# Optimization experiments

Measured on AMD Instinct MI355X. Metric: run time of the kernel, lower is better.

Reference implementation:

```python
import jax, jax.numpy as jnp
import numpy as np

N = 1024          # n_nodes
F = 32            # n_input_features (per-node embedding dim)
HID = 64          # n_hidden_features
OUT = 32          # n_output_features


def setup_inputs() -> dict:
    key = jax.random.key(0)
    k = jax.random.split(key, 7)
    Edges = jax.random.uniform(k[0], (N, N), dtype=jnp.float32)
    Coordinates = jax.random.normal(k[1], (N, 3), dtype=jnp.float32)
    Embeddings = jax.random.normal(k[2], (N, F), dtype=jnp.float32)
    # nn.Linear params: W (out, in), b (out,)
    s1 = 1.0 / np.sqrt(2 * F)
    s2 = 1.0 / np.sqrt(HID)
    W1 = jax.random.uniform(k[3], (HID, 2 * F), dtype=jnp.float32, minval=-s1, maxval=s1)
    b1 = jax.random.uniform(k[4], (HID,), dtype=jnp.float32, minval=-s1, maxval=s1)
    W2 = jax.random.uniform(k[5], (OUT, HID), dtype=jnp.float32, minval=-s2, maxval=s2)
    b2 = jax.random.uniform(k[6], (OUT,), dtype=jnp.float32, minval=-s2, maxval=s2)
    return {"Edges": Edges, "Coordinates": Coordinates, "Embeddings": Embeddings,
            "W1": W1, "b1": b1, "W2": W2, "b2": b2}


def _swish(x):
    return x * jax.nn.sigmoid(x)


def reference(Edges, Coordinates, Embeddings, W1, b1, W2, b2):
    # pairwise euclidean distances (torch.cdist p=2), grad-safe on the zero diagonal
    diff = Coordinates[:, None, :] - Coordinates[None, :, :]          # (N, N, 3)
    sq = jnp.sum(diff * diff, axis=-1)                                # (N, N)
    dist = jnp.where(sq > 0, jnp.sqrt(jnp.where(sq > 0, sq, 1.0)), 0.0)
    w = Edges * dist                                                  # (N, N)

    # H[i, j] = concat(Emb[i], Emb[j]); first Linear applied without
    # materializing the (N, N, 2F) tensor:
    # (w * [h_i, h_j]) @ W1^T = w * (h_i @ W1[:, :F]^T + h_j @ W1[:, F:]^T)
    A = Embeddings @ W1[:, :F].T                                      # (N, HID) from h_i half
    B = Embeddings @ W1[:, F:].T                                      # (N, HID) from h_j half
    pre1 = w[:, :, None] * (A[:, None, :] + B[None, :, :]) + b1       # (N, N, HID)
    h1 = _swish(pre1)
    pre2 = jnp.einsum('ijh,oh->ijo', h1, W2) + b2                     # (N, N, OUT)
    return _swish(pre2)                                               # squeeze() is a no-op (OUT > 1)
```

## Files before the change

### kernel.cpp

```cpp
#include <hip/hip_runtime.h>
#include <math.h>

#define NN   1024
#define FF   32
#define HID  64
#define OUTF 32
#define ITER 4

typedef unsigned int  uint;
typedef unsigned short ushort;
typedef __attribute__((ext_vector_type(8)))  __bf16 bf16x8;
typedef __attribute__((ext_vector_type(16))) float  floatx16;

#define WS_A    0
#define WS_B    (WS_A + NN*HID)
#define WS_C4   (WS_B + NN*HID)
#define WS_B1   (WS_C4 + NN*4)
#define WS_B2   (WS_B1 + HID)
#define WS_W2H  (WS_B2 + 64)
#define WS_W2L  (WS_W2H + 1024)

union FragU { ushort u[8]; bf16x8 v; };

__device__ __forceinline__ float swish(float x) {
    float e = __builtin_amdgcn_exp2f(x * -1.442695040888963f);
    return x * __builtin_amdgcn_rcpf(1.0f + e);
}

__global__ void prep_kernel(
    const float* __restrict__ Coords,
    const float* __restrict__ Emb,
    const float* __restrict__ W1,
    const float* __restrict__ b1,
    const float* __restrict__ W2,
    const float* __restrict__ b2,
    float* __restrict__ ws)
{
    const int b = blockIdx.x;
    const int t = threadIdx.x;
    if (b < NN) {
        float accA = 0.f, accB = 0.f;
        const float* w1row = W1 + t * (2 * FF);
        const float* erow  = Emb + b * FF;
        #pragma unroll
        for (int f = 0; f < FF; ++f) {
            float e = erow[f];
            accA = fmaf(e, w1row[f],      accA);
            accB = fmaf(e, w1row[FF + f], accB);
        }
        ws[WS_A + b * HID + t] = accA;
        ws[WS_B + b * HID + t] = accB;
    } else {
        if (t < HID)  ws[WS_B1 + t] = b1[t];
        if (t < OUTF) ws[WS_B2 + t] = b2[t];
        #pragma unroll 1
        for (int n = t; n < NN; n += 64) {
            ws[WS_C4 + n * 4 + 0] = Coords[n * 3 + 0];
            ws[WS_C4 + n * 4 + 1] = Coords[n * 3 + 1];
            ws[WS_C4 + n * 4 + 2] = Coords[n * 3 + 2];
            ws[WS_C4 + n * 4 + 3] = 0.f;
        }
        ushort* w2h = (ushort*)(ws + WS_W2H);
        ushort* w2l = (ushort*)(ws + WS_W2L);
        const int n  = t & 31;
        const int kh = (t >> 5) * 8;
        #pragma unroll
        for (int c = 0; c < 4; ++c) {
            #pragma unroll
            for (int j = 0; j < 8; ++j) {
                const int k = c * 16 + kh + j;
                const float v = W2[n * HID + k];
                const uint  x = __float_as_uint(v);
                const float lo = v - __uint_as_float(x & 0xffff0000u);
                w2h[(c * 64 + t) * 8 + j] = (ushort)(x >> 16);
                w2l[(c * 64 + t) * 8 + j] = (ushort)(__float_as_uint(lo) >> 16);
            }
        }
    }
}

__global__ __launch_bounds__(256) void main_kernel(
    const float* __restrict__ Edges,
    const float* __restrict__ ws,
    float* __restrict__ out)
{
    const int lane = threadIdx.x & 63;
    const int wave = threadIdx.x >> 6;
    const int j0   = blockIdx.x * 128 + wave * 32;
    const int i0   = blockIdx.y * ITER;
    const int p    = lane & 31;
    const int half = lane >> 5;
    const int jp   = j0 + p;

    const ushort* w2hp = (const ushort*)(ws + WS_W2H);
    const ushort* w2lp = (const ushort*)(ws + WS_W2L);
    bf16x8 bh[4], bl[4];
    #pragma unroll
    for (int c = 0; c < 4; ++c) {
        bh[c] = *(const bf16x8*)(w2hp + (c * 64 + lane) * 8);
        bl[c] = *(const bf16x8*)(w2lp + (c * 64 + lane) * 8);
    }
    const float* __restrict__ Bj  = ws + WS_B + jp * HID;
    const float* __restrict__ b1f = ws + WS_B1;
    float bv[4][8], b1v[4][8];
    #pragma unroll
    for (int c = 0; c < 4; ++c) {
        const int h0 = c * 16 + half * 8;
        *(float4*)(&bv[c][0])  = *(const float4*)(Bj + h0);
        *(float4*)(&bv[c][4])  = *(const float4*)(Bj + h0 + 4);
        *(float4*)(&b1v[c][0]) = *(const float4*)(b1f + h0);
        *(float4*)(&b1v[c][4]) = *(const float4*)(b1f + h0 + 4);
    }
    const float4 cj  = *(const float4*)(ws + WS_C4 + jp * 4);
    const float  b2n = ws[WS_B2 + p];

    #pragma unroll 1
    for (int it = 0; it < ITER; ++it) {
        const int i = i0 + it;

        const float cix = ws[WS_C4 + i * 4 + 0];
        const float ciy = ws[WS_C4 + i * 4 + 1];
        const float ciz = ws[WS_C4 + i * 4 + 2];
        const float dx = cix - cj.x, dy = ciy - cj.y, dz = ciz - cj.z;
        const float dist = sqrtf(dx * dx + dy * dy + dz * dz);
        const float w = Edges[(size_t)i * NN + jp] * dist;

        const float* __restrict__ Ai = ws + WS_A + (size_t)i * HID;

        FragU ah[4], al[4];
        #pragma unroll
        for (int c = 0; c < 4; ++c) {
            #pragma unroll
            for (int jj = 0; jj < 8; ++jj) {
                const float s_lo = Ai[c * 16 + jj];
                const float s_hi = Ai[c * 16 + 8 + jj];
                const float av   = half ? s_hi : s_lo;
                const float pre  = fmaf(w, av + bv[c][jj], b1v[c][jj]);
                const float h1   = swish(pre);
                const uint  x    = __float_as_uint(h1);
                const float lo   = h1 - __uint_as_float(x & 0xffff0000u);
                ah[c].u[jj] = (ushort)(x >> 16);
                al[c].u[jj] = (ushort)(__float_as_uint(lo) >> 16);
            }
        }

        floatx16 acc = {0.f,0.f,0.f,0.f,0.f,0.f,0.f,0.f,
                        0.f,0.f,0.f,0.f,0.f,0.f,0.f,0.f};
        #pragma unroll
        for (int c = 0; c < 4; ++c) {
            acc = __builtin_amdgcn_mfma_f32_32x32x16_bf16(ah[c].v, bh[c], acc, 0, 0, 0);
            acc = __builtin_amdgcn_mfma_f32_32x32x16_bf16(al[c].v, bh[c], acc, 0, 0, 0);
            acc = __builtin_amdgcn_mfma_f32_32x32x16_bf16(ah[c].v, bl[c], acc, 0, 0, 0);
        }

        float* __restrict__ ob = out + ((size_t)i * NN + j0) * OUTF + p;
        #pragma unroll
        for (int r = 0; r < 16; ++r) {
            const int m = (r & 3) + 8 * (r >> 2) + 4 * half;
            __builtin_nontemporal_store(swish(acc[r] + b2n), ob + m * OUTF);
        }
    }
}

extern "C" void kernel_launch(void* const* d_in, const int* in_sizes, int n_in,
                              void* d_out, int out_size, void* d_ws, size_t ws_size,
                              hipStream_t stream)
{
    const float* Edges  = (const float*)d_in[0];
    const float* Coords = (const float*)d_in[1];
    const float* Emb    = (const float*)d_in[2];
    const float* W1     = (const float*)d_in[3];
    const float* b1     = (const float*)d_in[4];
    const float* W2     = (const float*)d_in[5];
    const float* b2     = (const float*)d_in[6];
    float* ws  = (float*)d_ws;
    float* out = (float*)d_out;

    hipLaunchKernelGGL(prep_kernel, dim3(NN + 1), dim3(64), 0, stream,
                       Coords, Emb, W1, b1, W2, b2, ws);
    hipLaunchKernelGGL(main_kernel, dim3(NN / 128, NN / ITER), dim3(256), 0, stream,
                       Edges, ws, out);
}
```

Baseline: 193.6 us.

## Drop W2 low-part MFMA, stage A rows in LDS, double ITER, prefetch edges

W2 is now rounded to bf16 with round-to-nearest-even and its low-order residual fragment is removed, so the third MFMA in each chunk goes away. The per-row A values, b1 and the i-coordinates are staged once per block in LDS, replacing scalar global reads. ITER doubles to 8, launch bounds now ask for 4 blocks per CU, and the next Edges value is loaded one iteration ahead. This cuts the MFMA count and register pressure, at the cost of accuracy in the W2 product, and the larger ITER halves the number of blocks.

Measured after the change: 174.9 us. 1.11x faster.

```diff
diff --git a/kernel.cpp b/kernel.cpp
--- a/kernel.cpp
+++ b/kernel.cpp
@@ -5,7 +5,7 @@
 #define FF   32
 #define HID  64
 #define OUTF 32
-#define ITER 4
+#define ITER 8
 
 typedef unsigned int  uint;
 typedef unsigned short ushort;
@@ -18,13 +18,17 @@
 #define WS_B1   (WS_C4 + NN*4)
 #define WS_B2   (WS_B1 + HID)
 #define WS_W2H  (WS_B2 + 64)
-#define WS_W2L  (WS_W2H + 1024)
 
 union FragU { ushort u[8]; bf16x8 v; };
 
 __device__ __forceinline__ float swish(float x) {
     float e = __builtin_amdgcn_exp2f(x * -1.442695040888963f);
     return x * __builtin_amdgcn_rcpf(1.0f + e);
+}
+__device__ __forceinline__ ushort f2bf_rne(float f) {
+    uint x = __float_as_uint(f);
+    x += 0x7FFFu + ((x >> 16) & 1u);
+    return (ushort)(x >> 16);
 }
 
 __global__ void prep_kernel(
@@ -61,7 +65,6 @@
             ws[WS_C4 + n * 4 + 3] = 0.f;
         }
         ushort* w2h = (ushort*)(ws + WS_W2H);
-        ushort* w2l = (ushort*)(ws + WS_W2L);
         const int n  = t & 31;
         const int kh = (t >> 5) * 8;
         #pragma unroll
@@ -69,76 +72,89 @@
             #pragma unroll
             for (int j = 0; j < 8; ++j) {
                 const int k = c * 16 + kh + j;
-                const float v = W2[n * HID + k];
-                const uint  x = __float_as_uint(v);
-                const float lo = v - __uint_as_float(x & 0xffff0000u);
-                w2h[(c * 64 + t) * 8 + j] = (ushort)(x >> 16);
-                w2l[(c * 64 + t) * 8 + j] = (ushort)(__float_as_uint(lo) >> 16);
+                w2h[(c * 64 + t) * 8 + j] = f2bf_rne(W2[n * HID + k]);
             }
         }
     }
 }
 
-__global__ __launch_bounds__(256) void main_kernel(
+__global__ __launch_bounds__(256, 4) void main_kernel(
     const float* __restrict__ Edges,
     const float* __restrict__ ws,
     float* __restrict__ out)
 {
-    const int lane = threadIdx.x & 63;
-    const int wave = threadIdx.x >> 6;
+    __shared__ float lds[ITER * HID + HID + ITER * 4];
+
+    const int t    = threadIdx.x;
+    const int lane = t & 63;
+    const int wave = t >> 6;
     const int j0   = blockIdx.x * 128 + wave * 32;
     const int i0   = blockIdx.y * ITER;
     const int p    = lane & 31;
     const int half = lane >> 5;
     const int jp   = j0 + p;
 
+    {
+        const float* srcA = ws + WS_A + (size_t)i0 * HID;
+        if (t < 128) {
+            *(float4*)&lds[t * 4] = *(const float4*)(srcA + t * 4);
+        } else if (t < 144) {
+            *(float4*)&lds[ITER * HID + (t - 128) * 4] =
+                *(const float4*)(ws + WS_B1 + (t - 128) * 4);
+        } else if (t < 152) {
+            *(float4*)&lds[ITER * HID + HID + (t - 144) * 4] =
+                *(const float4*)(ws + WS_C4 + (size_t)(i0 + (t - 144)) * 4);
+        }
+    }
+
     const ushort* w2hp = (const ushort*)(ws + WS_W2H);
-    const ushort* w2lp = (const ushort*)(ws + WS_W2L);
-    bf16x8 bh[4], bl[4];
+    bf16x8 bh[4];
     #pragma unroll
-    for (int c = 0; c < 4; ++c) {
+    for (int c = 0; c < 4; ++c)
         bh[c] = *(const bf16x8*)(w2hp + (c * 64 + lane) * 8);
-        bl[c] = *(const bf16x8*)(w2lp + (c * 64 + lane) * 8);
-    }
-    const float* __restrict__ Bj  = ws + WS_B + jp * HID;
-    const float* __restrict__ b1f = ws + WS_B1;
-    float bv[4][8], b1v[4][8];
+
+    const float* __restrict__ Bj = ws + WS_B + (size_t)jp * HID;
+    float bv[4][8];
     #pragma unroll
     for (int c = 0; c < 4; ++c) {
         const int h0 = c * 16 + half * 8;
-        *(float4*)(&bv[c][0])  = *(const float4*)(Bj + h0);
-        *(float4*)(&bv[c][4])  = *(const float4*)(Bj + h0 + 4);
-        *(float4*)(&b1v[c][0]) = *(const float4*)(b1f + h0);
-        *(float4*)(&b1v[c][4]) = *(const float4*)(b1f + h0 + 4);
+        *(float4*)(&bv[c][0]) = *(const float4*)(Bj + h0);
+        *(float4*)(&bv[c][4]) = *(const float4*)(Bj + h0 + 4);
     }
-    const float4 cj  = *(const float4*)(ws + WS_C4 + jp * 4);
+    const float4 cj  = *(const float4*)(ws + WS_C4 + (size_t)jp * 4);
     const float  b2n = ws[WS_B2 + p];
+
+    __syncthreads();
+
+    const float* egp = Edges + (size_t)i0 * NN + jp;
+    float eg = *egp;
 
     #pragma unroll 1
     for (int it = 0; it < ITER; ++it) {
         const int i = i0 + it;
+        const float eg_cur = eg;
+        if (it + 1 < ITER) eg = egp[(size_t)(it + 1) * NN];
 
-        const float cix = ws[WS_C4 + i * 4 + 0];
-        const float ciy = ws[WS_C4 + i * 4 + 1];
-        const float ciz = ws[WS_C4 + i * 4 + 2];
-        const float dx = cix - cj.x, dy = ciy - cj.y, dz = ciz - cj.z;
+        const float4 civ = *(const float4*)&lds[ITER * HID + HID + it * 4];
+        const float dx = civ.x - cj.x, dy = civ.y - cj.y, dz = civ.z - cj.z;
         const float dist = sqrtf(dx * dx + dy * dy + dz * dz);
-        const float w = Edges[(size_t)i * NN + jp] * dist;
-
-        const float* __restrict__ Ai = ws + WS_A + (size_t)i * HID;
+        const float w = eg_cur * dist;
 
         FragU ah[4], al[4];
         #pragma unroll
         for (int c = 0; c < 4; ++c) {
+            const int ho = c * 16 + half * 8;
+            float av[8], b1c[8];
+            *(float4*)(av + 0)  = *(const float4*)&lds[it * HID + ho];
+            *(float4*)(av + 4)  = *(const float4*)&lds[it * HID + ho + 4];
+            *(float4*)(b1c + 0) = *(const float4*)&lds[ITER * HID + ho];
+            *(float4*)(b1c + 4) = *(const float4*)&lds[ITER * HID + ho + 4];
             #pragma unroll
             for (int jj = 0; jj < 8; ++jj) {
-                const float s_lo = Ai[c * 16 + jj];
-                const float s_hi = Ai[c * 16 + 8 + jj];
-                const float av   = half ? s_hi : s_lo;
-                const float pre  = fmaf(w, av + bv[c][jj], b1v[c][jj]);
-                const float h1   = swish(pre);
-                const uint  x    = __float_as_uint(h1);
-                const float lo   = h1 - __uint_as_float(x & 0xffff0000u);
+                const float pre = fmaf(w, av[jj] + bv[c][jj], b1c[jj]);
+                const float h1  = swish(pre);
+                const uint  x   = __float_as_uint(h1);
+                const float lo  = h1 - __uint_as_float(x & 0xffff0000u);
                 ah[c].u[jj] = (ushort)(x >> 16);
                 al[c].u[jj] = (ushort)(__float_as_uint(lo) >> 16);
             }
@@ -150,7 +166,6 @@
         for (int c = 0; c < 4; ++c) {
             acc = __builtin_amdgcn_mfma_f32_32x32x16_bf16(ah[c].v, bh[c], acc, 0, 0, 0);
             acc = __builtin_amdgcn_mfma_f32_32x32x16_bf16(al[c].v, bh[c], acc, 0, 0, 0);
-            acc = __builtin_amdgcn_mfma_f32_32x32x16_bf16(ah[c].v, bl[c], acc, 0, 0, 0);
         }
 
         float* __restrict__ ob = out + ((size_t)i * NN + j0) * OUTF + p;
```
